# Performance work log

Measured on AMD Instinct MI355X. Metric: run time of the kernel, lower is better.

Reference implementation:

```python
import jax, jax.numpy as jnp
import numpy as np

N = 100000      # nodes
E = 1600000     # edges (avg degree 16)
DIM = 128       # node_input_dim == node_hidden_dim
H = 8           # num_heads
D = DIM // H    # per-head out_feats = 16
NEG_SLOPE_ATTN = 0.2   # DGL GATConv attention LeakyReLU
NEG_SLOPE_ACT = 0.01   # F.leaky_relu default (inter-layer activation)


def _leaky(x, s):
    return jnp.where(x >= 0, x, s * x)


def setup_inputs() -> dict:
    key = jax.random.key(0)
    ks = jax.random.split(key, 12)
    s = 0.1
    return {
        "n_feat": jax.random.normal(ks[0], (N, DIM), jnp.float32),
        "src": jax.random.randint(ks[1], (E,), 0, N, dtype=jnp.int32),
        "dst": jax.random.randint(ks[2], (E,), 0, N, dtype=jnp.int32),
        # layer 0 params
        "W0": jax.random.normal(ks[3], (DIM, DIM), jnp.float32) * s,
        "al0": jax.random.normal(ks[4], (H, D), jnp.float32) * s,
        "ar0": jax.random.normal(ks[5], (H, D), jnp.float32) * s,
        "b0": jnp.zeros((DIM,), jnp.float32),
        # layer 1 params
        "W1": jax.random.normal(ks[6], (DIM, DIM), jnp.float32) * s,
        "al1": jax.random.normal(ks[7], (H, D), jnp.float32) * s,
        "ar1": jax.random.normal(ks[8], (H, D), jnp.float32) * s,
        "b1": jnp.zeros((DIM,), jnp.float32),
    }


def gat_layer(h, src, dst, W, al, ar, b, apply_act):
    # h: [N, DIM] -> feat: [N, H, D]
    feat = (h @ W).reshape(N, H, D)
    el = jnp.einsum('nhd,hd->nh', feat, al)   # [N, H]
    er = jnp.einsum('nhd,hd->nh', feat, ar)   # [N, H]
    # per-edge attention logits with LeakyReLU(0.2)
    e = _leaky(el[src] + er[dst], NEG_SLOPE_ATTN)         # [E, H]
    # edge-softmax over incoming edges of each dst node (numerically stable)
    m = jax.ops.segment_max(e, dst, num_segments=N)       # [N, H]
    ee = jnp.exp(e - m[dst])                              # [E, H]
    denom = jax.ops.segment_sum(ee, dst, num_segments=N)  # [N, H]
    a = ee / denom[dst]                                   # [E, H]
    # weighted message aggregation (scatter-add to dst)
    msg = feat[src] * a[:, :, None]                       # [E, H, D]
    rst = jax.ops.segment_sum(msg, dst, num_segments=N)   # [N, H, D]
    # residual (identity since in_feats == num_heads*out_feats) + bias
    rst = rst + h.reshape(N, H, D) + b.reshape(1, H, D)
    if apply_act:
        rst = _leaky(rst, NEG_SLOPE_ACT)
    return rst.reshape(N, H * D)


def reference(n_feat, src, dst, W0, al0, ar0, b0, W1, al1, ar1, b1):
    h = gat_layer(n_feat, src, dst, W0, al0, ar0, b0, apply_act=True)
    h = gat_layer(h, src, dst, W1, al1, ar1, b1, apply_act=False)
    return h
```

## Files before the change

kernel.cpp:

```cpp
#include <hip/hip_runtime.h>
#include <hip/hip_bf16.h>

#define HGAT 8
#define DIMGAT 128
#define CAPB 4608

typedef __attribute__((ext_vector_type(8))) short short8;
typedef __attribute__((ext_vector_type(4))) float f32x4;

__device__ __forceinline__ float bf16_to_f32(unsigned int u16) {
    return __uint_as_float(u16 << 16);
}
__device__ __forceinline__ unsigned short f32_to_bf16(float x) {
    unsigned int b = __float_as_uint(x);
    b += 0x7FFFu + ((b >> 16) & 1u);
    return (unsigned short)(b >> 16);
}

__global__ void initb_kernel(int* __restrict__ bcursor, int nb) {
    int i = blockIdx.x * blockDim.x + threadIdx.x;
    if (i < nb) bcursor[i] = i * CAPB;
}

__global__ __launch_bounds__(256)
void bucket_scatter(const int* __restrict__ src, const int* __restrict__ dst,
                    int* __restrict__ bcursor, unsigned int* __restrict__ bucket_arr,
                    int e, int nb) {
    __shared__ int lcnt[400];
    __shared__ int lbase[400];
    __shared__ int lrank[400];
    int t = threadIdx.x;
    int e0 = blockIdx.x * 4096;
    for (int i = t; i < nb; i += 256) { lcnt[i] = 0; lrank[i] = 0; }
    __syncthreads();
    int myb[16]; int mys[16];
    #pragma unroll
    for (int q = 0; q < 16; ++q) {
        int i = e0 + q * 256 + t;
        int bb = -1, ss = 0;
        if (i < e) {
            int d = dst[i];
            bb = d >> 8;
            ss = (src[i] << 8) | (d & 255);
        }
        myb[q] = bb; mys[q] = ss;
        if (bb >= 0) atomicAdd(&lcnt[bb], 1);
    }
    __syncthreads();
    for (int i = t; i < nb; i += 256) {
        int c = lcnt[i];
        lbase[i] = c ? atomicAdd(&bcursor[i], c) : 0;
    }
    __syncthreads();
    #pragma unroll
    for (int q = 0; q < 16; ++q) {
        int bb = myb[q];
        if (bb >= 0) {
            int r = atomicAdd(&lrank[bb], 1);
            int pos = lbase[bb] + r;
            if (pos < (bb + 1) * CAPB)
                bucket_arr[pos] = (unsigned int)mys[q];
        }
    }
}

__global__ __launch_bounds__(256)
void bucket_finalize(const unsigned int* __restrict__ bucket_arr,
                     const int* __restrict__ bcursor, int* __restrict__ col_src,
                     int* __restrict__ start, int* __restrict__ deg, int n) {
    __shared__ int lcnt[256];
    __shared__ int lcur[256];
    int b = blockIdx.x;
    int t = threadIdx.x;
    int base = b * CAPB;
    int cnt_b = bcursor[b] - base;
    lcnt[t] = 0;
    __syncthreads();
    for (int i = t; i < cnt_b; i += 256)
        atomicAdd(&lcnt[bucket_arr[base + i] & 255u], 1);
    __syncthreads();
    int my = lcnt[t];
    for (int off = 1; off < 256; off <<= 1) {
        int v = (t >= off) ? lcnt[t - off] : 0;
        __syncthreads();
        lcnt[t] += v;
        __syncthreads();
    }
    int excl = lcnt[t] - my;
    int node = b * 256 + t;
    if (node < n) {
        start[node] = base + excl;
        deg[node] = my;
    }
    lcur[t] = excl;
    __syncthreads();
    for (int i = t; i < cnt_b; i += 256) {
        unsigned int p = bucket_arr[base + i];
        int r = atomicAdd(&lcur[p & 255u], 1);
        col_src[base + r] = (int)(p >> 8);
    }
}

__global__ void wcvt_kernel(const float* __restrict__ W, unsigned short* __restrict__ Wb) {
    int t = blockIdx.x * blockDim.x + threadIdx.x;
    int lane = t & 63;
    int ct = (t >> 6) & 7;
    int ks = t >> 9;
    int lr = lane & 15, lg = lane >> 4;
    const float* wp = W + (ks * 32 + lg * 8) * 128 + ct * 16 + lr;
    unsigned short o[8];
    #pragma unroll
    for (int j = 0; j < 8; ++j) o[j] = f32_to_bf16(wp[j * 128]);
    *(uint4*)(Wb + (size_t)t * 8) = *(const uint4*)o;
}

__global__ __launch_bounds__(256)
void gemm_mfma_kernel(const float* __restrict__ A, const unsigned short* __restrict__ Wb,
                      unsigned short* __restrict__ Cb, int nrows) {
    int wave = (int)((blockIdx.x * (size_t)blockDim.x + threadIdx.x) >> 6);
    int nwaves = (int)((gridDim.x * (size_t)blockDim.x) >> 6);
    int lane = threadIdx.x & 63;
    int lr = lane & 15;
    int lg = lane >> 4;

    const short8* wb8 = (const short8*)Wb;
    short8 bfrag[4][8];
    #pragma unroll
    for (int ks = 0; ks < 4; ++ks)
        #pragma unroll
        for (int ct = 0; ct < 8; ++ct)
            bfrag[ks][ct] = wb8[(ks * 8 + ct) * 64 + lane];

    int ntiles = nrows >> 4;
    for (int t = wave; t < ntiles; t += nwaves) {
        const float* ap = A + (size_t)(t * 16 + lr) * 128 + lg * 8;
        f32x4 acc[8];
        #pragma unroll
        for (int ct = 0; ct < 8; ++ct) acc[ct] = (f32x4){0.f, 0.f, 0.f, 0.f};
        #pragma unroll
        for (int ks = 0; ks < 4; ++ks) {
            float4 a0 = *(const float4*)(ap + ks * 32);
            float4 a1 = *(const float4*)(ap + ks * 32 + 4);
            short8 af;
            af[0] = (short)f32_to_bf16(a0.x); af[1] = (short)f32_to_bf16(a0.y);
            af[2] = (short)f32_to_bf16(a0.z); af[3] = (short)f32_to_bf16(a0.w);
            af[4] = (short)f32_to_bf16(a1.x); af[5] = (short)f32_to_bf16(a1.y);
            af[6] = (short)f32_to_bf16(a1.z); af[7] = (short)f32_to_bf16(a1.w);
            #pragma unroll
            for (int ct = 0; ct < 8; ++ct)
                acc[ct] = __builtin_amdgcn_mfma_f32_16x16x32_bf16(af, bfrag[ks][ct], acc[ct], 0, 0, 0);
        }
        unsigned short* cp = Cb + (size_t)(t * 16 + lg * 4) * 128 + lr;
        #pragma unroll
        for (int ct = 0; ct < 8; ++ct) {
            #pragma unroll
            for (int r = 0; r < 4; ++r)
                cp[(size_t)r * 128 + ct * 16] = f32_to_bf16(acc[ct][r]);
        }
    }
}

__global__ void elr_kernel(const unsigned short* __restrict__ featb,
                           const float* __restrict__ al, const float* __restrict__ ar,
                           float* __restrict__ el, float* __restrict__ er, int n) {
    int idx = blockIdx.x * blockDim.x + threadIdx.x;
    if (idx >= n * HGAT) return;
    int h = idx & 7;
    const uint4* f4 = (const uint4*)(featb + (size_t)idx * 16);
    uint4 va = f4[0], vb = f4[1];
    unsigned int w[8] = {va.x, va.y, va.z, va.w, vb.x, vb.y, vb.z, vb.w};
    const float* a1 = al + h * 16;
    const float* a2 = ar + h * 16;
    float sl = 0.f, sr = 0.f;
    #pragma unroll
    for (int q = 0; q < 8; ++q) {
        float lo = bf16_to_f32(w[q] & 0xFFFFu);
        float hi = bf16_to_f32(w[q] >> 16);
        sl = fmaf(lo, a1[2 * q], fmaf(hi, a1[2 * q + 1], sl));
        sr = fmaf(lo, a2[2 * q], fmaf(hi, a2[2 * q + 1], sr));
    }
    el[idx] = sl;
    er[idx] = sr;
}

__global__ __launch_bounds__(256)
void agg_kernel(const unsigned short* __restrict__ featb, const float* __restrict__ el,
                const float* __restrict__ er, const int* __restrict__ col_src,
                const int* __restrict__ start_arr, const int* __restrict__ deg,
                const float* __restrict__ hin, const float* __restrict__ bias,
                float* __restrict__ out, int n, int applyAct) {
    int wid = (int)((blockIdx.x * (size_t)blockDim.x + threadIdx.x) >> 6);
    if (wid >= n) return;
    int lane = threadIdx.x & 63;
    int h = lane >> 3;
    int jbase = lane & 0x38;
    int start = start_arr[wid];
    int end = start + deg[wid];
    float er_own = er[wid * 8 + h];

    float sum = 0.f, ax = 0.f, ay = 0.f;
    const unsigned int* featw = (const unsigned int*)featb;
    int i = start;
    for (; i + 8 <= end; i += 8) {
        int s_own = col_src[i + (lane & 7)];
        float q = el[s_own * 8 + h] + er_own;
        q = (q >= 0.f) ? q : 0.2f * q;
        float p_own = __expf(q);
        #pragma unroll
        for (int j = 0; j < 8; ++j) {
            int sj   = __shfl(s_own, jbase + j);
            float pj = __shfl(p_own, jbase + j);
            sum += pj;
            unsigned int fw = featw[(size_t)sj * 64 + lane];
            ax = fmaf(pj, bf16_to_f32(fw & 0xFFFFu), ax);
            ay = fmaf(pj, bf16_to_f32(fw >> 16), ay);
        }
    }
    for (; i < end; ++i) {
        int s = col_src[i];
        float e = el[s * 8 + h] + er_own;
        e = (e >= 0.f) ? e : 0.2f * e;
        float p = __expf(e);
        sum += p;
        unsigned int fw = featw[(size_t)s * 64 + lane];
        ax = fmaf(p, bf16_to_f32(fw & 0xFFFFu), ax);
        ay = fmaf(p, bf16_to_f32(fw >> 16), ay);
    }
    float inv = (end > start) ? 1.f / sum : 0.f;
    float2 hv = ((const float2*)hin)[(size_t)wid * 64 + lane];
    float2 bv = ((const float2*)bias)[lane];
    float ox = fmaf(ax, inv, hv.x + bv.x);
    float oy = fmaf(ay, inv, hv.y + bv.y);
    if (applyAct) {
        ox = (ox >= 0.f) ? ox : 0.01f * ox;
        oy = (oy >= 0.f) ? oy : 0.01f * oy;
    }
    ((float2*)out)[(size_t)wid * 64 + lane] = make_float2(ox, oy);
}

extern "C" void kernel_launch(void* const* d_in, const int* in_sizes, int n_in,
                              void* d_out, int out_size, void* d_ws, size_t ws_size,
                              hipStream_t stream) {
    const float* n_feat = (const float*)d_in[0];
    const int*   src    = (const int*)d_in[1];
    const int*   dst    = (const int*)d_in[2];
    const float* W0  = (const float*)d_in[3];
    const float* al0 = (const float*)d_in[4];
    const float* ar0 = (const float*)d_in[5];
    const float* b0  = (const float*)d_in[6];
    const float* W1  = (const float*)d_in[7];
    const float* al1 = (const float*)d_in[8];
    const float* ar1 = (const float*)d_in[9];
    const float* b1  = (const float*)d_in[10];

    const int n = in_sizes[0] / DIMGAT;
    const int e = in_sizes[1];
    const int nb = (n + 255) >> 8;

    char* ws = (char*)d_ws;
    size_t off = 0;
    auto alloc = [&](size_t bytes) {
        void* p = ws + off;
        off += (bytes + 255) & ~(size_t)255;
        return p;
    };
    int* bcursor = (int*)alloc((size_t)nb * 4);
    int* start   = (int*)alloc((size_t)n * 4);
    int* deg     = (int*)alloc((size_t)n * 4);
    unsigned int* bucket_arr = (unsigned int*)alloc((size_t)nb * CAPB * 4);
    int* col_src = (int*)alloc((size_t)nb * CAPB * 4);
    float* el    = (float*)alloc((size_t)n * HGAT * 4);
    float* er    = (float*)alloc((size_t)n * HGAT * 4);
    unsigned short* featb = (unsigned short*)alloc((size_t)n * DIMGAT * 2);
    unsigned short* Wb    = (unsigned short*)alloc((size_t)DIMGAT * DIMGAT * 2);
    float* out   = (float*)d_out;

    initb_kernel<<<(nb + 255) / 256, 256, 0, stream>>>(bcursor, nb);
    bucket_scatter<<<(e + 4095) / 4096, 256, 0, stream>>>(src, dst, bcursor,
                                                          bucket_arr, e, nb);
    bucket_finalize<<<nb, 256, 0, stream>>>(bucket_arr, bcursor, col_src,
                                            start, deg, n);

    const int gemm_grid = 1024;
    const int elr_grid  = (n * HGAT + 255) / 256;
    const int agg_grid  = (n * 64 + 255) / 256;

    wcvt_kernel<<<8, 256, 0, stream>>>(W0, Wb);
    gemm_mfma_kernel<<<gemm_grid, 256, 0, stream>>>(n_feat, Wb, featb, n);
    elr_kernel<<<elr_grid, 256, 0, stream>>>(featb, al0, ar0, el, er, n);
    agg_kernel<<<agg_grid, 256, 0, stream>>>(featb, el, er, col_src, start, deg,
                                             n_feat, b0, out, n, 1);
    wcvt_kernel<<<8, 256, 0, stream>>>(W1, Wb);
    gemm_mfma_kernel<<<gemm_grid, 256, 0, stream>>>(out, Wb, featb, n);
    elr_kernel<<<elr_grid, 256, 0, stream>>>(featb, al1, ar1, el, er, n);
    agg_kernel<<<agg_grid, 256, 0, stream>>>(featb, el, er, col_src, start, deg,
                                             out, b1, out, n, 0);
}
```

Measured before the change: 388.2 us.

## Fuse attention logits into GEMM epilogue and store intermediate hidden state as bf16

Computes el/er directly from the MFMA accumulators in the GEMM epilogue using shuffle reductions, so the separate elr kernel and its re-read of the feature matrix go away. The layer-1 output is written as bf16 to a workspace buffer and read back by the second GEMM and residual, which halves that traffic. Both weight conversions are merged into one launch. In exchange the GEMM epilogue carries extra shuffles, and the residual path loses precision by rounding the hidden state to bf16.

```diff
diff --git a/kernel.cpp b/kernel.cpp
--- a/kernel.cpp
+++ b/kernel.cpp
@@ -101,22 +101,29 @@
     }
 }
 
-__global__ void wcvt_kernel(const float* __restrict__ W, unsigned short* __restrict__ Wb) {
+__global__ void wcvt_kernel(const float* __restrict__ W0, const float* __restrict__ W1,
+                            unsigned short* __restrict__ Wb0, unsigned short* __restrict__ Wb1) {
     int t = blockIdx.x * blockDim.x + threadIdx.x;
-    int lane = t & 63;
-    int ct = (t >> 6) & 7;
-    int ks = t >> 9;
+    const float* W = (t < 2048) ? W0 : W1;
+    unsigned short* Wb = (t < 2048) ? Wb0 : Wb1;
+    int tt = t & 2047;
+    int lane = tt & 63;
+    int ct = (tt >> 6) & 7;
+    int ks = tt >> 9;
     int lr = lane & 15, lg = lane >> 4;
     const float* wp = W + (ks * 32 + lg * 8) * 128 + ct * 16 + lr;
     unsigned short o[8];
     #pragma unroll
     for (int j = 0; j < 8; ++j) o[j] = f32_to_bf16(wp[j * 128]);
-    *(uint4*)(Wb + (size_t)t * 8) = *(const uint4*)o;
-}
-
+    *(uint4*)(Wb + (size_t)tt * 8) = *(const uint4*)o;
+}
+
+template<int AIN>
 __global__ __launch_bounds__(256)
-void gemm_mfma_kernel(const float* __restrict__ A, const unsigned short* __restrict__ Wb,
-                      unsigned short* __restrict__ Cb, int nrows) {
+void gemm_mfma_kernel(const void* __restrict__ A_, const unsigned short* __restrict__ Wb,
+                      unsigned short* __restrict__ Cb,
+                      const float* __restrict__ al, const float* __restrict__ ar,
+                      float* __restrict__ el, float* __restrict__ er, int nrows) {
     int wave = (int)((blockIdx.x * (size_t)blockDim.x + threadIdx.x) >> 6);
     int nwaves = (int)((gridDim.x * (size_t)blockDim.x) >> 6);
     int lane = threadIdx.x & 63;
@@ -131,21 +138,33 @@
         for (int ct = 0; ct < 8; ++ct)
             bfrag[ks][ct] = wb8[(ks * 8 + ct) * 64 + lane];
 
+    float alv[8], arv[8];
+    #pragma unroll
+    for (int ct = 0; ct < 8; ++ct) {
+        alv[ct] = al[ct * 16 + lr];
+        arv[ct] = ar[ct * 16 + lr];
+    }
+
     int ntiles = nrows >> 4;
     for (int t = wave; t < ntiles; t += nwaves) {
-        const float* ap = A + (size_t)(t * 16 + lr) * 128 + lg * 8;
         f32x4 acc[8];
         #pragma unroll
         for (int ct = 0; ct < 8; ++ct) acc[ct] = (f32x4){0.f, 0.f, 0.f, 0.f};
         #pragma unroll
         for (int ks = 0; ks < 4; ++ks) {
-            float4 a0 = *(const float4*)(ap + ks * 32);
-            float4 a1 = *(const float4*)(ap + ks * 32 + 4);
             short8 af;
-            af[0] = (short)f32_to_bf16(a0.x); af[1] = (short)f32_to_bf16(a0.y);
-            af[2] = (short)f32_to_bf16(a0.z); af[3] = (short)f32_to_bf16(a0.w);
-            af[4] = (short)f32_to_bf16(a1.x); af[5] = (short)f32_to_bf16(a1.y);
-            af[6] = (short)f32_to_bf16(a1.z); af[7] = (short)f32_to_bf16(a1.w);
+            if (AIN == 0) {
+                const float* ap = (const float*)A_ + (size_t)(t * 16 + lr) * 128 + lg * 8 + ks * 32;
+                float4 a0 = *(const float4*)ap;
+                float4 a1 = *(const float4*)(ap + 4);
+                af[0] = (short)f32_to_bf16(a0.x); af[1] = (short)f32_to_bf16(a0.y);
+                af[2] = (short)f32_to_bf16(a0.z); af[3] = (short)f32_to_bf16(a0.w);
+                af[4] = (short)f32_to_bf16(a1.x); af[5] = (short)f32_to_bf16(a1.y);
+                af[6] = (short)f32_to_bf16(a1.z); af[7] = (short)f32_to_bf16(a1.w);
+            } else {
+                const unsigned short* ap = (const unsigned short*)A_ + (size_t)(t * 16 + lr) * 128 + lg * 8 + ks * 32;
+                af = *(const short8*)ap;
+            }
             #pragma unroll
             for (int ct = 0; ct < 8; ++ct)
                 acc[ct] = __builtin_amdgcn_mfma_f32_16x16x32_bf16(af, bfrag[ks][ct], acc[ct], 0, 0, 0);
@@ -157,38 +176,34 @@
             for (int r = 0; r < 4; ++r)
                 cp[(size_t)r * 128 + ct * 16] = f32_to_bf16(acc[ct][r]);
         }
-    }
-}
-
-__global__ void elr_kernel(const unsigned short* __restrict__ featb,
-                           const float* __restrict__ al, const float* __restrict__ ar,
-                           float* __restrict__ el, float* __restrict__ er, int n) {
-    int idx = blockIdx.x * blockDim.x + threadIdx.x;
-    if (idx >= n * HGAT) return;
-    int h = idx & 7;
-    const uint4* f4 = (const uint4*)(featb + (size_t)idx * 16);
-    uint4 va = f4[0], vb = f4[1];
-    unsigned int w[8] = {va.x, va.y, va.z, va.w, vb.x, vb.y, vb.z, vb.w};
-    const float* a1 = al + h * 16;
-    const float* a2 = ar + h * 16;
-    float sl = 0.f, sr = 0.f;
-    #pragma unroll
-    for (int q = 0; q < 8; ++q) {
-        float lo = bf16_to_f32(w[q] & 0xFFFFu);
-        float hi = bf16_to_f32(w[q] >> 16);
-        sl = fmaf(lo, a1[2 * q], fmaf(hi, a1[2 * q + 1], sl));
-        sr = fmaf(lo, a2[2 * q], fmaf(hi, a2[2 * q + 1], sr));
-    }
-    el[idx] = sl;
-    er[idx] = sr;
-}
-
+        #pragma unroll
+        for (int r = 0; r < 4; ++r) {
+            int row = t * 16 + lg * 4 + r;
+            #pragma unroll
+            for (int ct = 0; ct < 8; ++ct) {
+                float vl = acc[ct][r] * alv[ct];
+                float vr = acc[ct][r] * arv[ct];
+                #pragma unroll
+                for (int off = 1; off < 16; off <<= 1) {
+                    vl += __shfl_xor(vl, off, 64);
+                    vr += __shfl_xor(vr, off, 64);
+                }
+                if (lr == 0) {
+                    el[(size_t)row * 8 + ct] = vl;
+                    er[(size_t)row * 8 + ct] = vr;
+                }
+            }
+        }
+    }
+}
+
+template<int HINB, int OUTB, int ACT>
 __global__ __launch_bounds__(256)
 void agg_kernel(const unsigned short* __restrict__ featb, const float* __restrict__ el,
                 const float* __restrict__ er, const int* __restrict__ col_src,
                 const int* __restrict__ start_arr, const int* __restrict__ deg,
-                const float* __restrict__ hin, const float* __restrict__ bias,
-                float* __restrict__ out, int n, int applyAct) {
+                const void* __restrict__ hin_, const float* __restrict__ bias,
+                void* __restrict__ out_, int n) {
     int wid = (int)((blockIdx.x * (size_t)blockDim.x + threadIdx.x) >> 6);
     if (wid >= n) return;
     int lane = threadIdx.x & 63;
@@ -227,15 +242,28 @@
         ay = fmaf(p, bf16_to_f32(fw >> 16), ay);
     }
     float inv = (end > start) ? 1.f / sum : 0.f;
-    float2 hv = ((const float2*)hin)[(size_t)wid * 64 + lane];
+    float hx, hy;
+    if (HINB) {
+        unsigned int hw = ((const unsigned int*)hin_)[(size_t)wid * 64 + lane];
+        hx = bf16_to_f32(hw & 0xFFFFu);
+        hy = bf16_to_f32(hw >> 16);
+    } else {
+        float2 hv = ((const float2*)hin_)[(size_t)wid * 64 + lane];
+        hx = hv.x; hy = hv.y;
+    }
     float2 bv = ((const float2*)bias)[lane];
-    float ox = fmaf(ax, inv, hv.x + bv.x);
-    float oy = fmaf(ay, inv, hv.y + bv.y);
-    if (applyAct) {
+    float ox = fmaf(ax, inv, hx + bv.x);
+    float oy = fmaf(ay, inv, hy + bv.y);
+    if (ACT) {
         ox = (ox >= 0.f) ? ox : 0.01f * ox;
         oy = (oy >= 0.f) ? oy : 0.01f * oy;
     }
-    ((float2*)out)[(size_t)wid * 64 + lane] = make_float2(ox, oy);
+    if (OUTB) {
+        unsigned int pw = (unsigned int)f32_to_bf16(ox) | ((unsigned int)f32_to_bf16(oy) << 16);
+        ((unsigned int*)out_)[(size_t)wid * 64 + lane] = pw;
+    } else {
+        ((float2*)out_)[(size_t)wid * 64 + lane] = make_float2(ox, oy);
+    }
 }
 
 extern "C" void kernel_launch(void* const* d_in, const int* in_sizes, int n_in,
@@ -272,27 +300,42 @@
     float* el    = (float*)alloc((size_t)n * HGAT * 4);
     float* er    = (float*)alloc((size_t)n * HGAT * 4);
     unsigned short* featb = (unsigned short*)alloc((size_t)n * DIMGAT * 2);
-    unsigned short* Wb    = (unsigned short*)alloc((size_t)DIMGAT * DIMGAT * 2);
-    float* out   = (float*)d_out;
+    unsigned short* Wb0   = (unsigned short*)alloc((size_t)DIMGAT * DIMGAT * 2);
+    unsigned short* Wb1   = (unsigned short*)alloc((size_t)DIMGAT * DIMGAT * 2);
+    size_t off_noh1 = off;
+    unsigned short* h1b   = (unsigned short*)alloc((size_t)n * DIMGAT * 2);
+    const bool useB = (off <= ws_size);
+    (void)off_noh1;
+
+    float* out = (float*)d_out;
 
     initb_kernel<<<(nb + 255) / 256, 256, 0, stream>>>(bcursor, nb);
     bucket_scatter<<<(e + 4095) / 4096, 256, 0, stream>>>(src, dst, bcursor,
                                                           bucket_arr, e, nb);
     bucket_finalize<<<nb, 256, 0, stream>>>(bucket_arr, bcursor, col_src,
                                             start, deg, n);
+    wcvt_kernel<<<16, 256, 0, stream>>>(W0, W1, Wb0, Wb1);
 
     const int gemm_grid = 1024;
-    const int elr_grid  = (n * HGAT + 255) / 256;
     const int agg_grid  = (n * 64 + 255) / 256;
 
-    wcvt_kernel<<<8, 256, 0, stream>>>(W0, Wb);
-    gemm_mfma_kernel<<<gemm_grid, 256, 0, stream>>>(n_feat, Wb, featb, n);
-    elr_kernel<<<elr_grid, 256, 0, stream>>>(featb, al0, ar0, el, er, n);
-    agg_kernel<<<agg_grid, 256, 0, stream>>>(featb, el, er, col_src, start, deg,
-                                             n_feat, b0, out, n, 1);
-    wcvt_kernel<<<8, 256, 0, stream>>>(W1, Wb);
-    gemm_mfma_kernel<<<gemm_grid, 256, 0, stream>>>(out, Wb, featb, n);
-    elr_kernel<<<elr_grid, 256, 0, stream>>>(featb, al1, ar1, el, er, n);
-    agg_kernel<<<agg_grid, 256, 0, stream>>>(featb, el, er, col_src, start, deg,
-                                             out, b1, out, n, 0);
-}
+    if (useB) {
+        gemm_mfma_kernel<0><<<gemm_grid, 256, 0, stream>>>(n_feat, Wb0, featb,
+                                                           al0, ar0, el, er, n);
+        agg_kernel<0, 1, 1><<<agg_grid, 256, 0, stream>>>(featb, el, er, col_src,
+                                                          start, deg, n_feat, b0, h1b, n);
+        gemm_mfma_kernel<1><<<gemm_grid, 256, 0, stream>>>(h1b, Wb1, featb,
+                                                           al1, ar1, el, er, n);
+        agg_kernel<1, 0, 0><<<agg_grid, 256, 0, stream>>>(featb, el, er, col_src,
+                                                          start, deg, h1b, b1, out, n);
+    } else {
+        gemm_mfma_kernel<0><<<gemm_grid, 256, 0, stream>>>(n_feat, Wb0, featb,
+                                                           al0, ar0, el, er, n);
+        agg_kernel<0, 0, 1><<<agg_grid, 256, 0, stream>>>(featb, el, er, col_src,
+                                                          start, deg, n_feat, b0, out, n);
+        gemm_mfma_kernel<0><<<gemm_grid, 256, 0, stream>>>(out, Wb1, featb,
+                                                           al1, ar1, el, er, n);
+        agg_kernel<0, 0, 0><<<agg_grid, 256, 0, stream>>>(featb, el, er, col_src,
+                                                          start, deg, out, b1, out, n);
+    }
+}
```

New measurement: 399.2 us. +2.8%, slower.
